# Optimization experiments

Hardware: AMD Instinct MI355X
Metric: run time of the kernel (lower is better)

## Reference

```python
import jax, jax.numpy as jnp
import numpy as np

N = 100_000          # nodes
E = 1_600_000        # directed edges (avg degree 16)
H = 128              # hidden_dim
OUT = 5              # output_dim (actions)
FOV = 11             # input_dim -> image side
LIN_IN = (FOV - 2) ** 2 * 3  # 243
LN_EPS = 1e-5


def _conv2d(x, w, b):
    # x: [N,3,h,w], w: [3,3,3,3] OIHW, VALID, stride 1
    y = jax.lax.conv_general_dilated(
        x, w, window_strides=(1, 1), padding='VALID',
        dimension_numbers=('NCHW', 'OIHW', 'NCHW'))
    return y + b[None, :, None, None]


def setup_inputs() -> dict:
    key = jax.random.key(0)
    ks = jax.random.split(key, 32)
    r = lambda i, shape, s=0.05: (jax.random.normal(ks[i], shape, jnp.float32) * s)
    inp = {
        'x': jax.random.normal(ks[0], (N, 3, FOV, FOV), jnp.float32),
        'edge_index': jax.random.randint(ks[1], (2, E), 0, N, jnp.int64)
                      if jax.config.jax_enable_x64 else
                      jax.random.randint(ks[1], (2, E), 0, N, jnp.int32),
        # CustomConv params
        'conv_w': r(2, (3, 3, 3, 3)), 'conv_b': r(3, (3,)),
        'conv_self_w': r(4, (3, 3, 3, 3)), 'conv_self_b': r(5, (3,)),
        'lin_w': r(6, (LIN_IN, H)), 'lin_b': r(7, (H,)),
        'lin_self_w': r(8, (LIN_IN, H)), 'lin_self_b': r(9, (H,)),
        # 3 SAGEConv layers: lin_l (aggregated, with bias), lin_r (root, no bias)
        'sage_lw': r(10, (3, H, H)), 'sage_lb': r(11, (3, H)),
        'sage_rw': r(12, (3, H, H)),
        # LayerNorms applied after layers 0,1,2
        'ln_g': jnp.ones((3, H), jnp.float32), 'ln_b': jnp.zeros((3, H), jnp.float32),
        # post_mp MLP (dropout is identity in eval)
        'mlp_w1': r(13, (H, H)), 'mlp_b1': r(14, (H,)),
        'mlp_w2': r(15, (H, OUT)), 'mlp_b2': r(16, (OUT,)),
    }
    return inp


def _layernorm(h, g, b):
    mu = jnp.mean(h, axis=-1, keepdims=True)
    var = jnp.var(h, axis=-1, keepdims=True)
    return (h - mu) * jax.lax.rsqrt(var + LN_EPS) * g + b


def reference(x, edge_index, conv_w, conv_b, conv_self_w, conv_self_b,
              lin_w, lin_b, lin_self_w, lin_self_b,
              sage_lw, sage_lb, sage_rw, ln_g, ln_b,
              mlp_w1, mlp_b1, mlp_w2, mlp_b2):
    src, dst = edge_index[0], edge_index[1]
    valid = (src != dst)  # remove_self_loops (CustomConv only)

    # ---- layer 0: CustomConv (add aggregation) ----
    self_x = jax.nn.relu(_conv2d(x, conv_self_w, conv_self_b).reshape(N, -1))
    self_x = self_x @ lin_self_w + lin_self_b              # [N,H]
    xn = jax.nn.relu(_conv2d(x, conv_w, conv_b).reshape(N, -1))
    xn = xn @ lin_w + lin_b                                # [N,H]
    msgs = xn[src] * valid[:, None].astype(xn.dtype)       # gather + mask self loops
    h = self_x + jax.ops.segment_sum(msgs, dst, num_segments=N)

    # SAGE mean-degree counts (all edges; SAGE does not remove self loops)
    cnt = jnp.maximum(
        jax.ops.segment_sum(jnp.ones((E,), h.dtype), dst, num_segments=N), 1.0)

    emb = h
    for i in range(4):
        if i > 0:
            j = i - 1
            agg = jax.ops.segment_sum(h[src], dst, num_segments=N) / cnt[:, None]
            h = agg @ sage_lw[j] + sage_lb[j] + h @ sage_rw[j]
        emb = h
        h = jax.nn.relu(h)            # dropout p=0.25 is identity in eval
        if i != 3:
            h = _layernorm(h, ln_g[i], ln_b[i])

    # task == 'node': no pooling
    logits = (h @ mlp_w1 + mlp_b1) @ mlp_w2 + mlp_b2
    return emb, jax.nn.log_softmax(logits, axis=1)
```

## Files before the change

kernel.cpp:

```cpp
#include <hip/hip_runtime.h>
#include <hip/hip_bf16.h>

typedef __hip_bfloat16 bf16;
typedef __attribute__((ext_vector_type(8))) short v8s;
typedef __attribute__((ext_vector_type(4))) float v4f;

#define N_NODES 100000
#define N_EDGES 1600000
#define LN_EPS 1e-5f

#define OFF_CONV_W      0
#define OFF_CONV_B      81
#define OFF_CONV_SW     84
#define OFF_CONV_SB     165
#define OFF_LIN_W       168
#define OFF_LIN_B       31272
#define OFF_LIN_SW      31400
#define OFF_LIN_SB      62504
#define OFF_SAGE_LW     62632
#define OFF_SAGE_LB     111784
#define OFF_SAGE_RW     112168
#define OFF_LN_G        161320
#define OFF_LN_B        161704
#define OFF_MLP_W1      162088
#define OFF_MLP_B1      178472
#define OFF_MLP_W2      178600
#define OFF_MLP_B2      179240
#define PARAM_TOTAL     179245

#define WTL_N 65536
#define WTS_N 98304
#define WTM_N 16384

__device__ __forceinline__ unsigned short f2b(float f) {
    bf16 h = __float2bfloat16(f);
    return __builtin_bit_cast(unsigned short, h);
}
__device__ __forceinline__ float blo(unsigned u) { return __uint_as_float(u << 16); }
__device__ __forceinline__ float bhi(unsigned u) { return __uint_as_float(u & 0xffff0000u); }
__device__ __forceinline__ unsigned pack2(float lo, float hi) {
    return (unsigned)f2b(lo) | ((unsigned)f2b(hi) << 16);
}

struct Ptr17 { const void* p[17]; };

__global__ void detect_kernel(const unsigned short* __restrict__ xw,
                              const unsigned int* __restrict__ ew,
                              int* __restrict__ flags) {
    __shared__ int sawBigExp, sawHigh;
    if (threadIdx.x == 0) { sawBigExp = 0; sawHigh = 0; }
    __syncthreads();
    int localBig = 0, localHigh = 0;
    for (int i = threadIdx.x; i < 65536; i += 256) {
        unsigned e = (xw[i] >> 7) & 0xFF;
        if (e >= 0xF0) localBig = 1;
    }
    for (int i = threadIdx.x; i < 8192; i += 256) {
        if (ew[2 * i + 1] != 0) localHigh = 1;
    }
    if (localBig) atomicOr(&sawBigExp, 1);
    if (localHigh) atomicOr(&sawHigh, 1);
    __syncthreads();
    if (threadIdx.x == 0) { flags[0] = sawBigExp; flags[1] = sawHigh ? 0 : 1; }
}

__global__ void cvt_params_kernel(Ptr17 ptrs, const int* __restrict__ flags,
                                  float* __restrict__ dst) {
    int i = blockIdx.x * 256 + threadIdx.x;
    if (i >= PARAM_TOTAL) return;
    const int ksz[17] = {81,3,81,3,31104,128,31104,128,49152,384,49152,384,384,16384,128,640,5};
    int seg = 0, off = i;
    while (off >= ksz[seg]) { off -= ksz[seg]; ++seg; }
    float v;
    if (flags[0]) v = ((const float*)ptrs.p[seg])[off];
    else          v = __bfloat162float(((const bf16*)ptrs.p[seg])[off]);
    dst[i] = v;
}

__global__ void cvt2_kernel(const float* __restrict__ P,
                            unsigned short* __restrict__ wtl,
                            unsigned short* __restrict__ wts,
                            unsigned short* __restrict__ wtm) {
    int i = blockIdx.x * 256 + threadIdx.x;
    if (i < WTL_N) {
        int f = i >> 8, k = i & 255;
        float v = 0.f;
        if (k < 243) v = (f < 128) ? P[OFF_LIN_W + k * 128 + f]
                                   : P[OFF_LIN_SW + k * 128 + (f - 128)];
        wtl[i] = f2b(v);
    } else if (i < WTL_N + WTS_N) {
        int j = i - WTL_N; int l = j >> 15; int r = j & 32767; int f = r >> 8; int k = r & 255;
        float v = (k < 128) ? P[OFF_SAGE_LW + l * 16384 + k * 128 + f]
                            : P[OFF_SAGE_RW + l * 16384 + (k - 128) * 128 + f];
        wts[j] = f2b(v);
    } else if (i < WTL_N + WTS_N + WTM_N) {
        int j = i - WTL_N - WTS_N; int f = j >> 7, k = j & 127;
        wtm[j] = f2b(P[OFF_MLP_W1 + k * 128 + f]);
    }
}

__global__ __launch_bounds__(320) void conv_lin_kernel(
    const void* __restrict__ x, const float* __restrict__ P,
    const unsigned short* __restrict__ wtl, const int* __restrict__ flags,
    unsigned short* __restrict__ xnb, float* __restrict__ selfh)
{
    __shared__ unsigned short xs[5808];
    __shared__ unsigned short ysb[16][2][256];
    __shared__ float wc[2][81];
    __shared__ float bc[2][3];
    int tid = threadIdx.x;
    int n0 = blockIdx.x * 16;

    if (tid < 81) { wc[0][tid] = P[OFF_CONV_W + tid]; wc[1][tid] = P[OFF_CONV_SW + tid]; }
    else if (tid < 84) { int o = tid - 81; bc[0][o] = P[OFF_CONV_B + o]; bc[1][o] = P[OFF_CONV_SB + o]; }

    for (int i = tid; i < 416; i += 320) {
        int j = i / 26, r2 = i % 26, p = r2 / 13, k = 243 + (r2 % 13);
        ysb[j][p][k] = 0;
    }

    if (flags[0]) {
        const float* xf = (const float*)x + (size_t)n0 * 363;
        for (int i = tid; i < 5808; i += 320) xs[i] = f2b(xf[i]);
    } else {
        const uint4* xsrc = (const uint4*)((const unsigned short*)x + (size_t)n0 * 363);
        uint4* xd = (uint4*)xs;
        for (int i = tid; i < 726; i += 320) xd[i] = xsrc[i];
    }
    __syncthreads();

    if (tid < 288) {
        int j = tid / 18, rem = tid % 18;
        int p = rem / 9, oi = rem % 9;
        float acc[27];
        #pragma unroll
        for (int o = 0; o < 3; o++) {
            float b = bc[p][o];
            #pragma unroll
            for (int oj = 0; oj < 9; oj++) acc[o * 9 + oj] = b;
        }
        #pragma unroll
        for (int c = 0; c < 3; c++) {
            #pragma unroll
            for (int ki = 0; ki < 3; ki++) {
                float xr[11];
                const unsigned short* row = &xs[j * 363 + c * 121 + (oi + ki) * 11];
                #pragma unroll
                for (int t = 0; t < 11; t++) xr[t] = blo(row[t]);
                #pragma unroll
                for (int o = 0; o < 3; o++) {
                    int wb = o * 27 + c * 9 + ki * 3;
                    float w0 = wc[p][wb], w1 = wc[p][wb + 1], w2 = wc[p][wb + 2];
                    #pragma unroll
                    for (int oj = 0; oj < 9; oj++)
                        acc[o * 9 + oj] += xr[oj] * w0 + xr[oj + 1] * w1 + xr[oj + 2] * w2;
                }
            }
        }
        #pragma unroll
        for (int o = 0; o < 3; o++)
            #pragma unroll
            for (int oj = 0; oj < 9; oj++)
                ysb[j][p][o * 81 + oi * 9 + oj] = f2b(fmaxf(acc[o * 9 + oj], 0.f));
    }
    __syncthreads();

    int wave = tid >> 6, lane = tid & 63, quad = lane >> 4, col = lane & 15;
    if (wave < 4) {
        int p = wave >> 1;
        v4f acc[4];
        #pragma unroll
        for (int t = 0; t < 4; t++) { acc[t][0] = 0.f; acc[t][1] = 0.f; acc[t][2] = 0.f; acc[t][3] = 0.f; }
        for (int s = 0; s < 8; s++) {
            int kq = s * 32 + quad * 8;
            v8s a = *(const v8s*)&ysb[col][p][kq];
            #pragma unroll
            for (int t = 0; t < 4; t++) {
                int f = (wave * 4 + t) * 16 + col;
                v8s b = *(const v8s*)&wtl[(size_t)f * 256 + kq];
                acc[t] = __builtin_amdgcn_mfma_f32_16x16x32_bf16(a, b, acc[t], 0, 0, 0);
            }
        }
        #pragma unroll
        for (int t = 0; t < 4; t++) {
            int f = (wave * 4 + t) * 16 + col;
            #pragma unroll
            for (int r = 0; r < 4; r++) {
                int node = n0 + quad * 4 + r;
                float v = acc[t][r];
                if (p == 0) xnb[(size_t)node * 128 + f] = f2b(v + P[OFF_LIN_B + f]);
                else        selfh[(size_t)node * 128 + (f - 128)] = v + P[OFF_LIN_SB + (f - 128)];
            }
        }
    }
}

__device__ __forceinline__ int ld_edge(const int* __restrict__ ew, size_t elem, int isi64) {
    size_t idx = isi64 ? (elem * 2) : elem;
    return ew[idx];
}

__global__ void degree_kernel(const int* __restrict__ ew, const int* __restrict__ flags,
                              int* __restrict__ deg) {
    int e = blockIdx.x * blockDim.x + threadIdx.x;
    if (e < N_EDGES) {
        int d = ld_edge(ew, (size_t)N_EDGES + e, flags[1]);
        if ((unsigned)d < N_NODES) atomicAdd(&deg[d], 1);
    }
}

__global__ __launch_bounds__(1024) void scanA(const int* __restrict__ deg, int* __restrict__ rowptr,
                                              float* __restrict__ cntf, int* __restrict__ bsum) {
    __shared__ int s[1024];
    int tid = threadIdx.x;
    int i = blockIdx.x * 1024 + tid;
    int v = (i < N_NODES) ? deg[i] : 0;
    s[tid] = v;
    __syncthreads();
    for (int off = 1; off < 1024; off <<= 1) {
        int t = (tid >= off) ? s[tid - off] : 0;
        __syncthreads();
        s[tid] += t;
        __syncthreads();
    }
    if (i < N_NODES) {
        rowptr[i] = s[tid] - v;
        cntf[i] = (float)(v < 1 ? 1 : v);
    }
    if (tid == 1023) bsum[blockIdx.x] = s[1023];
}

__global__ void scanB(const int* __restrict__ bsum, int* __restrict__ boff, int nb, int* __restrict__ rowptr_end) {
    if (threadIdx.x == 0 && blockIdx.x == 0) {
        int run = 0;
        for (int i = 0; i < nb; i++) { boff[i] = run; run += bsum[i]; }
        *rowptr_end = run;
    }
}

__global__ __launch_bounds__(1024) void scanC(int* __restrict__ rowptr, const int* __restrict__ boff,
                                              int* __restrict__ cursor) {
    int i = blockIdx.x * 1024 + threadIdx.x;
    if (i < N_NODES) {
        int v = rowptr[i] + boff[blockIdx.x];
        rowptr[i] = v;
        cursor[i] = v;
    }
}

__global__ void fill_kernel(const int* __restrict__ ew, const int* __restrict__ flags,
                            int* __restrict__ cursor, int* __restrict__ csr) {
    int e = blockIdx.x * blockDim.x + threadIdx.x;
    if (e < N_EDGES) {
        int isi64 = flags[1];
        int s = ld_edge(ew, (size_t)e, isi64);
        int d = ld_edge(ew, (size_t)N_EDGES + e, isi64);
        if ((unsigned)d < N_NODES) {
            int p = atomicAdd(&cursor[d], 1);
            if ((unsigned)p < N_EDGES)
                csr[p] = ((unsigned)s < N_NODES) ? (s | ((s == d) ? (int)0x80000000 : 0)) : -1;
        }
    }
}

__global__ __launch_bounds__(256) void agg0ln_kernel(const unsigned short* __restrict__ xnb,
        const float* __restrict__ selfh, const int* __restrict__ rowptr, const int* __restrict__ csr,
        const float* __restrict__ lng, const float* __restrict__ lnb,
        unsigned short* __restrict__ zb) {
    int wave = threadIdx.x >> 6, lane = threadIdx.x & 63;
    int g = lane >> 4, c = lane & 15;
    int n = blockIdx.x * 4 + wave;
    int beg = rowptr[n], end = rowptr[n + 1];
    float a[8];
    #pragma unroll
    for (int i = 0; i < 8; i++) a[i] = 0.f;
    const uint4* x4 = (const uint4*)xnb;
    for (int b = beg; b < end; b += 64) {
        int bl = b + lane;
        int my = (bl < end) ? csr[bl] : -1;
        int nb = end - b; if (nb > 64) nb = 64;
        for (int i = 0; i < nb; i += 16) {
            int sv0 = __shfl(my, i + g, 64);
            int sv1 = __shfl(my, i + 4 + g, 64);
            int sv2 = __shfl(my, i + 8 + g, 64);
            int sv3 = __shfl(my, i + 12 + g, 64);
            bool va0 = ((unsigned)sv0 < N_NODES);
            bool va1 = ((unsigned)sv1 < N_NODES);
            bool va2 = ((unsigned)sv2 < N_NODES);
            bool va3 = ((unsigned)sv3 < N_NODES);
            uint4 v0 = x4[(size_t)(va0 ? sv0 : 0) * 16 + c];
            uint4 v1 = x4[(size_t)(va1 ? sv1 : 0) * 16 + c];
            uint4 v2 = x4[(size_t)(va2 ? sv2 : 0) * 16 + c];
            uint4 v3 = x4[(size_t)(va3 ? sv3 : 0) * 16 + c];
            if (va0) {
                a[0] += blo(v0.x); a[1] += bhi(v0.x);
                a[2] += blo(v0.y); a[3] += bhi(v0.y);
                a[4] += blo(v0.z); a[5] += bhi(v0.z);
                a[6] += blo(v0.w); a[7] += bhi(v0.w);
            }
            if (va1) {
                a[0] += blo(v1.x); a[1] += bhi(v1.x);
                a[2] += blo(v1.y); a[3] += bhi(v1.y);
                a[4] += blo(v1.z); a[5] += bhi(v1.z);
                a[6] += blo(v1.w); a[7] += bhi(v1.w);
            }
            if (va2) {
                a[0] += blo(v2.x); a[1] += bhi(v2.x);
                a[2] += blo(v2.y); a[3] += bhi(v2.y);
                a[4] += blo(v2.z); a[5] += bhi(v2.z);
                a[6] += blo(v2.w); a[7] += bhi(v2.w);
            }
            if (va3) {
                a[0] += blo(v3.x); a[1] += bhi(v3.x);
                a[2] += blo(v3.y); a[3] += bhi(v3.y);
                a[4] += blo(v3.z); a[5] += bhi(v3.z);
                a[6] += blo(v3.w); a[7] += bhi(v3.w);
            }
        }
    }
    #pragma unroll
    for (int i = 0; i < 8; i++) {
        a[i] += __shfl_xor(a[i], 16, 64);
        a[i] += __shfl_xor(a[i], 32, 64);
    }
    if (g == 0) {
        const float4* s4 = (const float4*)(selfh + (size_t)n * 128 + c * 8);
        float4 s0 = s4[0], s1 = s4[1];
        float v[8];
        v[0] = s0.x + a[0]; v[1] = s0.y + a[1]; v[2] = s0.z + a[2]; v[3] = s0.w + a[3];
        v[4] = s1.x + a[4]; v[5] = s1.y + a[5]; v[6] = s1.z + a[6]; v[7] = s1.w + a[7];
        float s = 0.f, sq = 0.f;
        #pragma unroll
        for (int i = 0; i < 8; i++) {
            v[i] = fmaxf(v[i], 0.f);
            s += v[i]; sq += v[i] * v[i];
        }
        #pragma unroll
        for (int m = 8; m >= 1; m >>= 1) {
            s  += __shfl_xor(s, m, 64);
            sq += __shfl_xor(sq, m, 64);
        }
        float mu = s * (1.f / 128.f);
        float var = sq * (1.f / 128.f) - mu * mu;
        float is = rsqrtf(var + LN_EPS);
        const float4* g4 = (const float4*)(lng + c * 8);
        const float4* b4 = (const float4*)(lnb + c * 8);
        float4 g0 = g4[0], g1 = g4[1], b0 = b4[0], b1 = b4[1];
        float z[8];
        z[0] = (v[0] - mu) * is * g0.x + b0.x; z[1] = (v[1] - mu) * is * g0.y + b0.y;
        z[2] = (v[2] - mu) * is * g0.z + b0.z; z[3] = (v[3] - mu) * is * g0.w + b0.w;
        z[4] = (v[4] - mu) * is * g1.x + b1.x; z[5] = (v[5] - mu) * is * g1.y + b1.y;
        z[6] = (v[6] - mu) * is * g1.z + b1.z; z[7] = (v[7] - mu) * is * g1.w + b1.w;
        uint4 o;
        o.x = pack2(z[0], z[1]); o.y = pack2(z[2], z[3]);
        o.z = pack2(z[4], z[5]); o.w = pack2(z[6], z[7]);
        ((uint4*)zb)[(size_t)n * 16 + c] = o;
    }
}

__global__ __launch_bounds__(256) void sagefused_kernel(
        const unsigned short* __restrict__ cur,
        const int* __restrict__ rowptr, const int* __restrict__ csr,
        const float* __restrict__ cntf, const unsigned short* __restrict__ wts,
        const float* __restrict__ lb, const float* __restrict__ lng, const float* __restrict__ lnb,
        int last, unsigned short* __restrict__ nxt, float* __restrict__ hout) {
    __shared__ unsigned short al[16][128];
    __shared__ float hb[16][128];
    int tid = threadIdx.x;
    int n0 = blockIdx.x * 16;
    int wave = tid >> 6, lane = tid & 63;
    int g = lane >> 4, c = lane & 15;
    const uint4* z4 = (const uint4*)cur;

    for (int q = 0; q < 4; q++) {
        int jj = wave * 4 + q;
        int n = n0 + jj;
        int beg = rowptr[n], end = rowptr[n + 1];
        float a[8];
        #pragma unroll
        for (int i = 0; i < 8; i++) a[i] = 0.f;
        for (int b = beg; b < end; b += 64) {
            int bl = b + lane;
            int my = (bl < end) ? csr[bl] : -1;
            int nb = end - b; if (nb > 64) nb = 64;
            for (int i = 0; i < nb; i += 16) {
                int sv0 = __shfl(my, i + g, 64) & 0x7fffffff;
                int sv1 = __shfl(my, i + 4 + g, 64) & 0x7fffffff;
                int sv2 = __shfl(my, i + 8 + g, 64) & 0x7fffffff;
                int sv3 = __shfl(my, i + 12 + g, 64) & 0x7fffffff;
                bool va0 = (sv0 < N_NODES);
                bool va1 = (sv1 < N_NODES);
                bool va2 = (sv2 < N_NODES);
                bool va3 = (sv3 < N_NODES);
                uint4 v0 = z4[(size_t)(va0 ? sv0 : 0) * 16 + c];
                uint4 v1 = z4[(size_t)(va1 ? sv1 : 0) * 16 + c];
                uint4 v2 = z4[(size_t)(va2 ? sv2 : 0) * 16 + c];
                uint4 v3 = z4[(size_t)(va3 ? sv3 : 0) * 16 + c];
                if (va0) {
                    a[0] += blo(v0.x); a[1] += bhi(v0.x);
                    a[2] += blo(v0.y); a[3] += bhi(v0.y);
                    a[4] += blo(v0.z); a[5] += bhi(v0.z);
                    a[6] += blo(v0.w); a[7] += bhi(v0.w);
                }
                if (va1) {
                    a[0] += blo(v1.x); a[1] += bhi(v1.x);
                    a[2] += blo(v1.y); a[3] += bhi(v1.y);
                    a[4] += blo(v1.z); a[5] += bhi(v1.z);
                    a[6] += blo(v1.w); a[7] += bhi(v1.w);
                }
                if (va2) {
                    a[0] += blo(v2.x); a[1] += bhi(v2.x);
                    a[2] += blo(v2.y); a[3] += bhi(v2.y);
                    a[4] += blo(v2.z); a[5] += bhi(v2.z);
                    a[6] += blo(v2.w); a[7] += bhi(v2.w);
                }
                if (va3) {
                    a[0] += blo(v3.x); a[1] += bhi(v3.x);
                    a[2] += blo(v3.y); a[3] += bhi(v3.y);
                    a[4] += blo(v3.z); a[5] += bhi(v3.z);
                    a[6] += blo(v3.w); a[7] += bhi(v3.w);
                }
            }
        }
        #pragma unroll
        for (int i = 0; i < 8; i++) {
            a[i] += __shfl_xor(a[i], 16, 64);
            a[i] += __shfl_xor(a[i], 32, 64);
        }
        if (g == 0) {
            float inv = 1.f / cntf[n];
            uint4 o;
            o.x = pack2(a[0] * inv, a[1] * inv); o.y = pack2(a[2] * inv, a[3] * inv);
            o.z = pack2(a[4] * inv, a[5] * inv); o.w = pack2(a[6] * inv, a[7] * inv);
            ((uint4*)&al[jj][0])[c] = o;
        }
    }
    __syncthreads();

    int quad = g, col = c;
    int nodeA = n0 + col;
    v4f acc[2];
    #pragma unroll
    for (int t = 0; t < 2; t++) { acc[t][0] = 0.f; acc[t][1] = 0.f; acc[t][2] = 0.f; acc[t][3] = 0.f; }
    #pragma unroll
    for (int s = 0; s < 8; s++) {
        int kq = s * 32 + quad * 8;
        const unsigned short* abase = (s < 4) ? &al[col][kq]
                                              : (cur + (size_t)nodeA * 128 + (kq - 128));
        v8s a = *(const v8s*)abase;
        #pragma unroll
        for (int t = 0; t < 2; t++) {
            int f = (wave * 2 + t) * 16 + col;
            v8s b = *(const v8s*)&wts[(size_t)f * 256 + kq];
            acc[t] = __builtin_amdgcn_mfma_f32_16x16x32_bf16(a, b, acc[t], 0, 0, 0);
        }
    }
    #pragma unroll
    for (int t = 0; t < 2; t++) {
        int f = (wave * 2 + t) * 16 + col;
        float bias = lb[f];
        #pragma unroll
        for (int r = 0; r < 4; r++)
            hb[quad * 4 + r][f] = acc[t][r] + bias;
    }
    __syncthreads();

    #pragma unroll
    for (int jj = 0; jj < 4; jj++) {
        int j = wave * 4 + jj;
        int node = n0 + j;
        float v0 = hb[j][2 * lane], v1 = hb[j][2 * lane + 1];
        if (last) {
            float2 w; w.x = v0; w.y = v1;
            ((float2*)hout)[(size_t)node * 64 + lane] = w;
        } else {
            float r0 = fmaxf(v0, 0.f), r1 = fmaxf(v1, 0.f);
            float s = r0 + r1, sq = r0 * r0 + r1 * r1;
            #pragma unroll
            for (int m = 32; m >= 1; m >>= 1) {
                s  += __shfl_xor(s, m, 64);
                sq += __shfl_xor(sq, m, 64);
            }
            float mu = s * (1.f / 128.f);
            float var = sq * (1.f / 128.f) - mu * mu;
            float inv = rsqrtf(var + LN_EPS);
            float z0 = (r0 - mu) * inv * lng[2 * lane]     + lnb[2 * lane];
            float z1 = (r1 - mu) * inv * lng[2 * lane + 1] + lnb[2 * lane + 1];
            ((unsigned int*)nxt)[(size_t)node * 64 + lane] = pack2(z0, z1);
        }
    }
}

__global__ __launch_bounds__(256) void mlp_kernel(const float* __restrict__ h,
        const unsigned short* __restrict__ wtm, const float* __restrict__ P,
        const int* __restrict__ flags, void* __restrict__ out) {
    __shared__ unsigned short rb[16][128];
    __shared__ float mb[16][128];
    __shared__ float lg[16][5];
    int tid = threadIdx.x;
    int n0 = blockIdx.x * 16;
    int isf = flags[0];

    const float2* h2 = (const float2*)h;
    for (int i = tid; i < 16 * 64; i += 256) {
        int j = i >> 6, q = i & 63;
        float2 v = h2[(size_t)(n0 + j) * 64 + q];
        size_t oi = (size_t)(n0 + j) * 128 + 2 * q;
        if (isf) { ((float*)out)[oi] = v.x; ((float*)out)[oi + 1] = v.y; }
        else ((unsigned int*)out)[oi >> 1] = pack2(v.x, v.y);
        rb[j][2 * q]     = f2b(fmaxf(v.x, 0.f));
        rb[j][2 * q + 1] = f2b(fmaxf(v.y, 0.f));
    }
    __syncthreads();

    int wave = tid >> 6, lane = tid & 63, quad = lane >> 4, col = lane & 15;
    v4f acc[2];
    #pragma unroll
    for (int t = 0; t < 2; t++) { acc[t][0] = 0.f; acc[t][1] = 0.f; acc[t][2] = 0.f; acc[t][3] = 0.f; }
    #pragma unroll
    for (int s = 0; s < 4; s++) {
        int kq = s * 32 + quad * 8;
        v8s a = *(const v8s*)&rb[col][kq];
        #pragma unroll
        for (int t = 0; t < 2; t++) {
            int f = (wave * 2 + t) * 16 + col;
            v8s b = *(const v8s*)&wtm[(size_t)f * 128 + kq];
            acc[t] = __builtin_amdgcn_mfma_f32_16x16x32_bf16(a, b, acc[t], 0, 0, 0);
        }
    }
    #pragma unroll
    for (int t = 0; t < 2; t++) {
        int f = (wave * 2 + t) * 16 + col;
        float bias = P[OFF_MLP_B1 + f];
        #pragma unroll
        for (int r = 0; r < 4; r++)
            mb[quad * 4 + r][f] = acc[t][r] + bias;
    }
    __syncthreads();

    if (tid < 80) {
        int j = tid / 5, o = tid - (tid / 5) * 5;
        float a = P[OFF_MLP_B2 + o];
        for (int k = 0; k < 128; k++) a += mb[j][k] * P[OFF_MLP_W2 + k * 5 + o];
        lg[j][o] = a;
    }
    __syncthreads();
    if (tid < 16) {
        int j = tid;
        float mx = lg[j][0];
        #pragma unroll
        for (int o = 1; o < 5; o++) mx = fmaxf(mx, lg[j][o]);
        float se = 0.f;
        #pragma unroll
        for (int o = 0; o < 5; o++) se += expf(lg[j][o] - mx);
        float lse = mx + logf(se);
        size_t base = (size_t)N_NODES * 128 + (size_t)(n0 + j) * 5;
        #pragma unroll
        for (int o = 0; o < 5; o++) {
            float v = lg[j][o] - lse;
            if (isf) ((float*)out)[base + o] = v;
            else     ((bf16*)out)[base + o] = __float2bfloat16(v);
        }
    }
}

extern "C" void kernel_launch(void* const* d_in, const int* in_sizes, int n_in,
                              void* d_out, int out_size, void* d_ws, size_t ws_size,
                              hipStream_t stream) {
    const void* x  = d_in[0];
    const int*  ew = (const int*)d_in[1];

    Ptr17 ptrs;
    for (int i = 0; i < 17; i++) ptrs.p[i] = d_in[2 + i];

    char* w = (char*)d_ws;
    auto carve = [&](size_t bytes) { char* r = w; w += (bytes + 255) & ~(size_t)255; return r; };
    float*          bufS  = (float*)carve((size_t)N_NODES * 128 * 4);
    unsigned short* xnb   = (unsigned short*)carve((size_t)N_NODES * 128 * 2);
    unsigned short* zb    = (unsigned short*)carve((size_t)N_NODES * 128 * 2);
    unsigned short* aggb  = (unsigned short*)carve((size_t)N_NODES * 128 * 2);
    float*          pf32  = (float*)carve((size_t)PARAM_TOTAL * 4);
    unsigned short* wtl   = (unsigned short*)carve((size_t)WTL_N * 2);
    unsigned short* wts   = (unsigned short*)carve((size_t)WTS_N * 2);
    unsigned short* wtm   = (unsigned short*)carve((size_t)WTM_N * 2);
    int*   deg    = (int*)carve((size_t)N_NODES * 4);
    int*   rowptr = (int*)carve((size_t)(N_NODES + 64) * 4);
    int*   cursor = (int*)carve((size_t)N_NODES * 4);
    float* cntf   = (float*)carve((size_t)N_NODES * 4);
    int*   bsum   = (int*)carve(512);
    int*   boff   = (int*)carve(512);
    int*   flags  = (int*)carve(256);
    int*   csr    = (int*)carve((size_t)N_EDGES * 4);

    const int SCAN_BLOCKS = (N_NODES + 1023) / 1024;

    detect_kernel<<<1, 256, 0, stream>>>((const unsigned short*)x, (const unsigned int*)ew, flags);
    cvt_params_kernel<<<(PARAM_TOTAL + 255) / 256, 256, 0, stream>>>(ptrs, flags, pf32);
    cvt2_kernel<<<(WTL_N + WTS_N + WTM_N + 255) / 256, 256, 0, stream>>>(pf32, wtl, wts, wtm);

    hipMemsetAsync(deg, 0, (size_t)N_NODES * 4, stream);

    conv_lin_kernel<<<N_NODES / 16, 320, 0, stream>>>(x, pf32, wtl, flags, xnb, bufS);

    degree_kernel<<<(N_EDGES + 255) / 256, 256, 0, stream>>>(ew, flags, deg);
    scanA<<<SCAN_BLOCKS, 1024, 0, stream>>>(deg, rowptr, cntf, bsum);
    scanB<<<1, 1, 0, stream>>>(bsum, boff, SCAN_BLOCKS, rowptr + N_NODES);
    scanC<<<SCAN_BLOCKS, 1024, 0, stream>>>(rowptr, boff, cursor);
    fill_kernel<<<(N_EDGES + 255) / 256, 256, 0, stream>>>(ew, flags, cursor, csr);

    agg0ln_kernel<<<N_NODES / 4, 256, 0, stream>>>(xnb, bufS, rowptr, csr,
        pf32 + OFF_LN_G, pf32 + OFF_LN_B, zb);

    unsigned short* cur = zb;
    unsigned short* nxt = aggb;
    for (int l = 0; l < 3; l++) {
        sagefused_kernel<<<N_NODES / 16, 256, 0, stream>>>(cur, rowptr, csr, cntf,
            wts + (size_t)l * 32768,
            pf32 + OFF_SAGE_LB + l * 128,
            pf32 + OFF_LN_G + (l + 1) * 128, pf32 + OFF_LN_B + (l + 1) * 128,
            (l == 2) ? 1 : 0, nxt, bufS);
        unsigned short* t = cur; cur = nxt; nxt = t;
    }

    mlp_kernel<<<N_NODES / 16, 256, 0, stream>>>(bufS, wtm, pf32, flags, d_out);
}
```

Measured before the change: 1.087 ms.

## Fuse degree counting into conv kernel and fuse last SAGE layer with MLP

```diff
diff --git a/kernel.cpp b/kernel.cpp
--- a/kernel.cpp
+++ b/kernel.cpp
@@ -31,6 +31,9 @@
 #define WTL_N 65536
 #define WTS_N 98304
 #define WTM_N 16384
+
+#define CONV_BLOCKS 6250
+#define DEG_BLOCKS  6250
 
 __device__ __forceinline__ unsigned short f2b(float f) {
     bf16 h = __float2bfloat16(f);
@@ -99,11 +102,29 @@
     }
 }
 
-__global__ __launch_bounds__(320) void conv_lin_kernel(
+__device__ __forceinline__ int ld_edge(const int* __restrict__ ew, size_t elem, int isi64) {
+    size_t idx = isi64 ? (elem * 2) : elem;
+    return ew[idx];
+}
+
+__global__ __launch_bounds__(320) void conv_deg_kernel(
     const void* __restrict__ x, const float* __restrict__ P,
     const unsigned short* __restrict__ wtl, const int* __restrict__ flags,
+    const int* __restrict__ ew, int* __restrict__ deg,
     unsigned short* __restrict__ xnb, float* __restrict__ selfh)
 {
+    if (blockIdx.x >= CONV_BLOCKS) {
+        int tid = threadIdx.x;
+        if (tid < 256) {
+            int e = (blockIdx.x - CONV_BLOCKS) * 256 + tid;
+            if (e < N_EDGES) {
+                int d = ld_edge(ew, (size_t)N_EDGES + e, flags[1]);
+                if ((unsigned)d < N_NODES) atomicAdd(&deg[d], 1);
+            }
+        }
+        return;
+    }
+
     __shared__ unsigned short xs[5808];
     __shared__ unsigned short ysb[16][2][256];
     __shared__ float wc[2][81];
@@ -192,20 +213,6 @@
                 else        selfh[(size_t)node * 128 + (f - 128)] = v + P[OFF_LIN_SB + (f - 128)];
             }
         }
-    }
-}
-
-__device__ __forceinline__ int ld_edge(const int* __restrict__ ew, size_t elem, int isi64) {
-    size_t idx = isi64 ? (elem * 2) : elem;
-    return ew[idx];
-}
-
-__global__ void degree_kernel(const int* __restrict__ ew, const int* __restrict__ flags,
-                              int* __restrict__ deg) {
-    int e = blockIdx.x * blockDim.x + threadIdx.x;
-    if (e < N_EDGES) {
-        int d = ld_edge(ew, (size_t)N_EDGES + e, flags[1]);
-        if ((unsigned)d < N_NODES) atomicAdd(&deg[d], 1);
     }
 }
 
@@ -358,20 +365,11 @@
     }
 }
 
-__global__ __launch_bounds__(256) void sagefused_kernel(
-        const unsigned short* __restrict__ cur,
+__device__ __forceinline__ void sage_gather(const unsigned short* __restrict__ cur,
         const int* __restrict__ rowptr, const int* __restrict__ csr,
-        const float* __restrict__ cntf, const unsigned short* __restrict__ wts,
-        const float* __restrict__ lb, const float* __restrict__ lng, const float* __restrict__ lnb,
-        int last, unsigned short* __restrict__ nxt, float* __restrict__ hout) {
-    __shared__ unsigned short al[16][128];
-    __shared__ float hb[16][128];
-    int tid = threadIdx.x;
-    int n0 = blockIdx.x * 16;
-    int wave = tid >> 6, lane = tid & 63;
-    int g = lane >> 4, c = lane & 15;
+        const float* __restrict__ cntf, int n0, int wave, int lane, int g, int c,
+        unsigned short al[16][128]) {
     const uint4* z4 = (const uint4*)cur;
-
     for (int q = 0; q < 4; q++) {
         int jj = wave * 4 + q;
         int n = n0 + jj;
@@ -435,6 +433,22 @@
             ((uint4*)&al[jj][0])[c] = o;
         }
     }
+}
+
+__global__ __launch_bounds__(256) void sagefused_kernel(
+        const unsigned short* __restrict__ cur,
+        const int* __restrict__ rowptr, const int* __restrict__ csr,
+        const float* __restrict__ cntf, const unsigned short* __restrict__ wts,
+        const float* __restrict__ lb, const float* __restrict__ lng, const float* __restrict__ lnb,
+        unsigned short* __restrict__ nxt) {
+    __shared__ unsigned short al[16][128];
+    __shared__ float hb[16][128];
+    int tid = threadIdx.x;
+    int n0 = blockIdx.x * 16;
+    int wave = tid >> 6, lane = tid & 63;
+    int g = lane >> 4, c = lane & 15;
+
+    sage_gather(cur, rowptr, csr, cntf, n0, wave, lane, g, c, al);
     __syncthreads();
 
     int quad = g, col = c;
@@ -470,53 +484,85 @@
         int j = wave * 4 + jj;
         int node = n0 + j;
         float v0 = hb[j][2 * lane], v1 = hb[j][2 * lane + 1];
-        if (last) {
-            float2 w; w.x = v0; w.y = v1;
-            ((float2*)hout)[(size_t)node * 64 + lane] = w;
-        } else {
-            float r0 = fmaxf(v0, 0.f), r1 = fmaxf(v1, 0.f);
-            float s = r0 + r1, sq = r0 * r0 + r1 * r1;
-            #pragma unroll
-            for (int m = 32; m >= 1; m >>= 1) {
-                s  += __shfl_xor(s, m, 64);
-                sq += __shfl_xor(sq, m, 64);
-            }
-            float mu = s * (1.f / 128.f);
-            float var = sq * (1.f / 128.f) - mu * mu;
-            float inv = rsqrtf(var + LN_EPS);
-            float z0 = (r0 - mu) * inv * lng[2 * lane]     + lnb[2 * lane];
-            float z1 = (r1 - mu) * inv * lng[2 * lane + 1] + lnb[2 * lane + 1];
-            ((unsigned int*)nxt)[(size_t)node * 64 + lane] = pack2(z0, z1);
-        }
-    }
-}
-
-__global__ __launch_bounds__(256) void mlp_kernel(const float* __restrict__ h,
-        const unsigned short* __restrict__ wtm, const float* __restrict__ P,
-        const int* __restrict__ flags, void* __restrict__ out) {
+        float r0 = fmaxf(v0, 0.f), r1 = fmaxf(v1, 0.f);
+        float s = r0 + r1, sq = r0 * r0 + r1 * r1;
+        #pragma unroll
+        for (int m = 32; m >= 1; m >>= 1) {
+            s  += __shfl_xor(s, m, 64);
+            sq += __shfl_xor(sq, m, 64);
+        }
+        float mu = s * (1.f / 128.f);
+        float var = sq * (1.f / 128.f) - mu * mu;
+        float inv = rsqrtf(var + LN_EPS);
+        float z0 = (r0 - mu) * inv * lng[2 * lane]     + lnb[2 * lane];
+        float z1 = (r1 - mu) * inv * lng[2 * lane + 1] + lnb[2 * lane + 1];
+        ((unsigned int*)nxt)[(size_t)node * 64 + lane] = pack2(z0, z1);
+    }
+}
+
+__global__ __launch_bounds__(256) void sagemlp_kernel(
+        const unsigned short* __restrict__ cur,
+        const int* __restrict__ rowptr, const int* __restrict__ csr,
+        const float* __restrict__ cntf, const unsigned short* __restrict__ wts,
+        const float* __restrict__ lb, const unsigned short* __restrict__ wtm,
+        const float* __restrict__ P, const int* __restrict__ flags,
+        void* __restrict__ out) {
+    __shared__ unsigned short al[16][128];
+    __shared__ float hb[16][128];
     __shared__ unsigned short rb[16][128];
     __shared__ float mb[16][128];
     __shared__ float lg[16][5];
     int tid = threadIdx.x;
     int n0 = blockIdx.x * 16;
+    int wave = tid >> 6, lane = tid & 63;
+    int g = lane >> 4, c = lane & 15;
     int isf = flags[0];
 
-    const float2* h2 = (const float2*)h;
+    sage_gather(cur, rowptr, csr, cntf, n0, wave, lane, g, c, al);
+    __syncthreads();
+
+    int quad = g, col = c;
+    int nodeA = n0 + col;
+    v4f acc[2];
+    #pragma unroll
+    for (int t = 0; t < 2; t++) { acc[t][0] = 0.f; acc[t][1] = 0.f; acc[t][2] = 0.f; acc[t][3] = 0.f; }
+    #pragma unroll
+    for (int s = 0; s < 8; s++) {
+        int kq = s * 32 + quad * 8;
+        const unsigned short* abase = (s < 4) ? &al[col][kq]
+                                              : (cur + (size_t)nodeA * 128 + (kq - 128));
+        v8s a = *(const v8s*)abase;
+        #pragma unroll
+        for (int t = 0; t < 2; t++) {
+            int f = (wave * 2 + t) * 16 + col;
+            v8s b = *(const v8s*)&wts[(size_t)f * 256 + kq];
+            acc[t] = __builtin_amdgcn_mfma_f32_16x16x32_bf16(a, b, acc[t], 0, 0, 0);
+        }
+    }
+    #pragma unroll
+    for (int t = 0; t < 2; t++) {
+        int f = (wave * 2 + t) * 16 + col;
+        float bias = lb[f];
+        #pragma unroll
+        for (int r = 0; r < 4; r++)
+            hb[quad * 4 + r][f] = acc[t][r] + bias;
+    }
+    __syncthreads();
+
     for (int i = tid; i < 16 * 64; i += 256) {
         int j = i >> 6, q = i & 63;
-        float2 v = h2[(size_t)(n0 + j) * 64 + q];
+        float vx = hb[j][2 * q], vy = hb[j][2 * q + 1];
         size_t oi = (size_t)(n0 + j) * 128 + 2 * q;
-        if (isf) { ((float*)out)[oi] = v.x; ((float*)out)[oi + 1] = v.y; }
-        else ((unsigned int*)out)[oi >> 1] = pack2(v.x, v.y);
-        rb[j][2 * q]     = f2b(fmaxf(v.x, 0.f));
-        rb[j][2 * q + 1] = f2b(fmaxf(v.y, 0.f));
-    }
-    __syncthreads();
-
-    int wave = tid >> 6, lane = tid & 63, quad = lane >> 4, col = lane & 15;
-    v4f acc[2];
-    #pragma unroll
-    for (int t = 0; t < 2; t++) { acc[t][0] = 0.f; acc[t][1] = 0.f; acc[t][2] = 0.f; acc[t][3] = 0.f; }
+        if (isf) { ((float*)out)[oi] = vx; ((float*)out)[oi + 1] = vy; }
+        else ((unsigned int*)out)[oi >> 1] = pack2(vx, vy);
+        rb[j][2 * q]     = f2b(fmaxf(vx, 0.f));
+        rb[j][2 * q + 1] = f2b(fmaxf(vy, 0.f));
+    }
+    __syncthreads();
+
+    v4f acc2[2];
+    #pragma unroll
+    for (int t = 0; t < 2; t++) { acc2[t][0] = 0.f; acc2[t][1] = 0.f; acc2[t][2] = 0.f; acc2[t][3] = 0.f; }
     #pragma unroll
     for (int s = 0; s < 4; s++) {
         int kq = s * 32 + quad * 8;
@@ -525,7 +571,7 @@
         for (int t = 0; t < 2; t++) {
             int f = (wave * 2 + t) * 16 + col;
             v8s b = *(const v8s*)&wtm[(size_t)f * 128 + kq];
-            acc[t] = __builtin_amdgcn_mfma_f32_16x16x32_bf16(a, b, acc[t], 0, 0, 0);
+            acc2[t] = __builtin_amdgcn_mfma_f32_16x16x32_bf16(a, b, acc2[t], 0, 0, 0);
         }
     }
     #pragma unroll
@@ -534,7 +580,7 @@
         float bias = P[OFF_MLP_B1 + f];
         #pragma unroll
         for (int r = 0; r < 4; r++)
-            mb[quad * 4 + r][f] = acc[t][r] + bias;
+            mb[quad * 4 + r][f] = acc2[t][r] + bias;
     }
     __syncthreads();
 
@@ -600,9 +646,9 @@
 
     hipMemsetAsync(deg, 0, (size_t)N_NODES * 4, stream);
 
-    conv_lin_kernel<<<N_NODES / 16, 320, 0, stream>>>(x, pf32, wtl, flags, xnb, bufS);
-
-    degree_kernel<<<(N_EDGES + 255) / 256, 256, 0, stream>>>(ew, flags, deg);
+    conv_deg_kernel<<<CONV_BLOCKS + DEG_BLOCKS, 320, 0, stream>>>(x, pf32, wtl, flags,
+        ew, deg, xnb, bufS);
+
     scanA<<<SCAN_BLOCKS, 1024, 0, stream>>>(deg, rowptr, cntf, bsum);
     scanB<<<1, 1, 0, stream>>>(bsum, boff, SCAN_BLOCKS, rowptr + N_NODES);
     scanC<<<SCAN_BLOCKS, 1024, 0, stream>>>(rowptr, boff, cursor);
@@ -611,16 +657,12 @@
     agg0ln_kernel<<<N_NODES / 4, 256, 0, stream>>>(xnb, bufS, rowptr, csr,
         pf32 + OFF_LN_G, pf32 + OFF_LN_B, zb);
 
-    unsigned short* cur = zb;
-    unsigned short* nxt = aggb;
-    for (int l = 0; l < 3; l++) {
-        sagefused_kernel<<<N_NODES / 16, 256, 0, stream>>>(cur, rowptr, csr, cntf,
-            wts + (size_t)l * 32768,
-            pf32 + OFF_SAGE_LB + l * 128,
-            pf32 + OFF_LN_G + (l + 1) * 128, pf32 + OFF_LN_B + (l + 1) * 128,
-            (l == 2) ? 1 : 0, nxt, bufS);
-        unsigned short* t = cur; cur = nxt; nxt = t;
-    }
-
-    mlp_kernel<<<N_NODES / 16, 256, 0, stream>>>(bufS, wtm, pf32, flags, d_out);
-}
+    sagefused_kernel<<<N_NODES / 16, 256, 0, stream>>>(zb, rowptr, csr, cntf,
+        wts, pf32 + OFF_SAGE_LB,
+        pf32 + OFF_LN_G + 128, pf32 + OFF_LN_B + 128, aggb);
+    sagefused_kernel<<<N_NODES / 16, 256, 0, stream>>>(aggb, rowptr, csr, cntf,
+        wts + 32768, pf32 + OFF_SAGE_LB + 128,
+        pf32 + OFF_LN_G + 256, pf32 + OFF_LN_B + 256, zb);
+    sagemlp_kernel<<<N_NODES / 16, 256, 0, stream>>>(zb, rowptr, csr, cntf,
+        wts + 65536, pf32 + OFF_SAGE_LB + 256, wtm, pf32, flags, d_out);
+}
```

Result: faster. 1.048 ms (-3.6%).
